# Performance work log

Measured on AMD Instinct MI355X. Metric: run time of the kernel, lower is better.

Reference implementation:

```python
import jax, jax.numpy as jnp
import numpy as np

N_NODES = 8192
N_GRAPHS = 16
KNN_K = 80
N_FEAT = 6
KNN_COLS = (0, 1, 2, 3)
HID = 128
HID6 = 6 * HID
N_LABELS = 3
BN_EPS = 1e-5


def knn_edges(pos, batch, k):
    # pos: [N, 4]; batch: [N] graph ids. Returns (src, tgt) with k neighbors per node,
    # restricted to same graph, excluding self (PyG knn_graph, flow source_to_target).
    n = pos.shape[0]
    sq = jnp.sum(pos * pos, axis=1)
    d2 = sq[:, None] + sq[None, :] - 2.0 * (pos @ pos.T)  # [N, N]
    valid = (batch[:, None] == batch[None, :]) & ~jnp.eye(n, dtype=bool)
    d2 = jnp.where(valid, d2, jnp.inf)
    _, idx = jax.lax.top_k(-d2, k)  # k smallest distances per row
    src = idx.reshape(-1)                      # neighbor j (message source)
    tgt = jnp.repeat(jnp.arange(n), k)         # center node i (message target)
    return src, tgt


def tag_conv(x, src, tgt, norm, W, b):
    # TAGConv K=2: out = sum_k (A_hat^k x) W_k + b, A_hat = D^-1/2 A D^-1/2
    n = x.shape[0]
    out = x @ W[0]
    h = x
    for k in range(1, W.shape[0]):
        h = jax.ops.segment_sum(norm[:, None] * h[src], tgt, num_segments=n)
        out = out + h @ W[k]
    return out + b


def pool_mean_max(x, batch, n_graphs):
    cnt = jax.ops.segment_sum(jnp.ones((x.shape[0],), x.dtype), batch, num_segments=n_graphs)
    mean = jax.ops.segment_sum(x, batch, num_segments=n_graphs) / cnt[:, None]
    mx = jax.ops.segment_max(x, batch, num_segments=n_graphs)
    return jnp.concatenate([mean, mx], axis=1)


def setup_inputs() -> dict:
    key = jax.random.key(0)
    ks = jax.random.split(key, 16)
    x = jax.random.normal(ks[0], (N_NODES, N_FEAT), dtype=jnp.float32)
    batch = jnp.repeat(jnp.arange(N_GRAPHS, dtype=jnp.int32), N_NODES // N_GRAPHS)
    s1 = 1.0 / np.sqrt(N_FEAT)
    s2 = 1.0 / np.sqrt(HID)
    s3 = 1.0 / np.sqrt(HID6)
    return {
        "x": x,
        "batch": batch,
        "conv1_w": jax.random.uniform(ks[1], (3, N_FEAT, HID), jnp.float32, -s1, s1),
        "conv1_b": jnp.zeros((HID,), jnp.float32),
        "conv2_w": jax.random.uniform(ks[2], (3, HID, HID), jnp.float32, -s2, s2),
        "conv2_b": jnp.zeros((HID,), jnp.float32),
        "conv3_w": jax.random.uniform(ks[3], (3, HID, HID), jnp.float32, -s2, s2),
        "conv3_b": jnp.zeros((HID,), jnp.float32),
        "bn_gamma": jnp.ones((HID6,), jnp.float32),
        "bn_beta": jnp.zeros((HID6,), jnp.float32),
        "bn_mean": 0.1 * jax.random.normal(ks[4], (HID6,), jnp.float32),
        "bn_var": jax.random.uniform(ks[5], (HID6,), jnp.float32, 0.5, 1.5),
        "lin_w": jax.random.uniform(ks[6], (5, HID6, HID6), jnp.float32, -s3, s3),
        "lin_b": jax.random.uniform(ks[7], (5, HID6), jnp.float32, -s3, s3),
        "out_w": jax.random.uniform(ks[8], (HID6, N_LABELS), jnp.float32, -s3, s3),
        "out_b": jax.random.uniform(ks[9], (N_LABELS,), jnp.float32, -s3, s3),
    }


def reference(x, batch, conv1_w, conv1_b, conv2_w, conv2_b, conv3_w, conv3_b,
              bn_gamma, bn_beta, bn_mean, bn_var, lin_w, lin_b, out_w, out_b):
    n = x.shape[0]
    pos = x[:, jnp.array(KNN_COLS)]
    src, tgt = knn_edges(pos, batch, KNN_K)
    # gcn_norm without self loops (edge dropout disabled: eval-mode determinism)
    deg = jax.ops.segment_sum(jnp.ones_like(src, dtype=x.dtype), tgt, num_segments=n)
    dinv = jnp.where(deg > 0, jax.lax.rsqrt(jnp.maximum(deg, 1.0)), 0.0)
    norm = dinv[src] * dinv[tgt]

    h = jax.nn.leaky_relu(tag_conv(x, src, tgt, norm, conv1_w, conv1_b))
    p1 = pool_mean_max(h, batch, N_GRAPHS)
    h = jax.nn.leaky_relu(tag_conv(h, src, tgt, norm, conv2_w, conv2_b))
    p2 = pool_mean_max(h, batch, N_GRAPHS)
    h = jax.nn.leaky_relu(tag_conv(h, src, tgt, norm, conv3_w, conv3_b))
    p3 = pool_mean_max(h, batch, N_GRAPHS)

    g = jnp.concatenate([p1, p2, p3], axis=1)  # [B, 768]
    g = (g - bn_mean) * jax.lax.rsqrt(bn_var + BN_EPS) * bn_gamma + bn_beta
    for i in range(lin_w.shape[0]):
        g = jax.nn.leaky_relu(g @ lin_w[i] + lin_b[i])
    out = g @ out_w + out_b
    return out.reshape(-1, N_LABELS)
```

## Files before the change

kernel.cpp:

```cpp
#include <hip/hip_runtime.h>

constexpr int N    = 8192;
constexpr int NPG  = 512;
constexpr int NG   = 16;
constexpr int KNN  = 80;
constexpr int F0   = 6;
constexpr int HID  = 128;
constexpr int H6   = 768;
constexpr int RPB  = 16;
constexpr int BPGR = NPG / RPB;


__device__ __forceinline__ float leaky(float v) { return v > 0.0f ? v : 0.01f * v; }

__device__ __forceinline__ int lanes_below(unsigned long long m) {
    return __builtin_amdgcn_mbcnt_hi((unsigned)(m >> 32),
           __builtin_amdgcn_mbcnt_lo((unsigned)m, 0));
}

__device__ __forceinline__ int wave_count_sum(int c) {
    int total = 0;
    #pragma unroll
    for (int b = 0; b < 4; b++)
        total += (int)__popcll(__ballot((c >> b) & 1)) << b;
    return total;
}

__global__ __launch_bounds__(256) void knn_kernel(const float* __restrict__ x,
                                                  int* __restrict__ nbr) {
    const int bid   = blockIdx.x;
    const int slot  = bid & 7;
    const int idx   = bid >> 3;
    const int g     = slot + 8 * (idx >> 7);
    const int chunk = idx & 127;
    const int tid  = threadIdx.x;
    const int lane = tid & 63;
    const int wv   = tid >> 6;
    const int base = g << 9;
    const int tl   = chunk * 4 + wv;
    const int t    = base + tl;

    __shared__ float px[512], py[512], pz[512], pw[512];
    __shared__ unsigned long long skey[4 * 128];

    for (int j = tid; j < 512; j += 256) {
        const float* row = x + (size_t)(base + j) * F0;
        const float2 ra = *(const float2*)(row);
        const float2 rb = *(const float2*)(row + 2);
        px[j] = ra.x; py[j] = ra.y; pz[j] = rb.x; pw[j] = rb.y;
    }
    __syncthreads();

    const float tx = px[tl], ty = py[tl], tz = pz[tl], tw = pw[tl];
    const float sqt = tx*tx + ty*ty + tz*tz + tw*tw;

    unsigned d2m[8];
    #pragma unroll
    for (int j = 0; j < 8; j++) {
        const int node = j * 64 + lane;
        const float jx = px[node], jy = py[node], jz = pz[node], jw = pw[node];
        const float sqj = jx*jx + jy*jy + jz*jz + jw*jw;
        const float dot = tx*jx + ty*jy + tz*jz + tw*jw;
        const float d2  = sqt + sqj - 2.0f * dot;
        unsigned u = __float_as_uint(d2);
        u = (u & 0x80000000u) ? ~u : (u | 0x80000000u);
        d2m[j] = (node == tl) ? 0xFFFFFFFFu : u;
    }

    unsigned V = 0;
    for (int b = 31; b >= 0; --b) {
        const unsigned test = V | (1u << b);
        int c = 0;
        #pragma unroll
        for (int j = 0; j < 8; j++) c += (d2m[j] < test) ? 1 : 0;
        if (wave_count_sum(c) < KNN) V = test;
    }

    int c = 0;
    #pragma unroll
    for (int j = 0; j < 8; j++) c += (d2m[j] < V) ? 1 : 0;
    const int n_lt = wave_count_sum(c);
    const int need = KNN - n_lt;

    const int woff = wv * 128;
    int cnt_total = 0, taken = 0;
    #pragma unroll
    for (int j = 0; j < 8; j++) {
        const bool lt = d2m[j] < V;
        const bool eq = d2m[j] == V;
        const unsigned long long meq = __ballot(eq);
        const bool sel = lt || (eq && (taken + lanes_below(meq)) < need);
        taken += (int)__popcll(meq);
        const unsigned long long msel = __ballot(sel);
        if (sel) {
            const int pos = cnt_total + lanes_below(msel);
            skey[woff + pos] = ((unsigned long long)d2m[j] << 32)
                             | (unsigned)(base + j * 64 + lane);
        }
        cnt_total += (int)__popcll(msel);
    }
    for (int i = KNN + lane; i < 128; i += 64) skey[woff + i] = ~0ULL;
    __syncthreads();

    for (int kk = 2; kk <= 128; kk <<= 1) {
        for (int jj = kk >> 1; jj >= 1; jj >>= 1) {
            const int i  = ((lane & ~(jj - 1)) << 1) | (lane & (jj - 1));
            const int ix = i | jj;
            const unsigned long long a = skey[woff + i];
            const unsigned long long b = skey[woff + ix];
            const bool up = ((i & kk) == 0);
            if ((a > b) == up) { skey[woff + i] = b; skey[woff + ix] = a; }
            __syncthreads();
        }
    }

    if (lane < KNN)      nbr[t * KNN + lane]      = (int)(unsigned)skey[woff + lane];
    if (lane + 64 < KNN) nbr[t * KNN + lane + 64] = (int)(unsigned)skey[woff + lane + 64];
}

__global__ __launch_bounds__(256) void prop6(const float* __restrict__ hin,
                                             const int* __restrict__ nbr,
                                             float* __restrict__ hout) {
    const int bid   = blockIdx.x;
    const int slot  = bid & 7;
    const int idx   = bid >> 3;
    const int g     = slot + 8 * (idx >> 4);
    const int chunk = idx & 15;
    const int t     = (g << 9) + chunk * 32 + (threadIdx.x >> 3);
    const int sl    = threadIdx.x & 7;
    const int* nb   = nbr + t * KNN + sl * 10;

    float a[F0] = {0.f, 0.f, 0.f, 0.f, 0.f, 0.f};
    #pragma unroll
    for (int j = 0; j < 10; j++) {
        const float* r = hin + (size_t)nb[j] * F0;
        #pragma unroll
        for (int f = 0; f < F0; f++) a[f] += r[f];
    }
    #pragma unroll
    for (int off = 1; off < 8; off <<= 1)
        #pragma unroll
        for (int f = 0; f < F0; f++) a[f] += __shfl_xor(a[f], off);

    if (sl == 0) {
        const float inv = 1.0f / 80.0f;
        float* o = hout + (size_t)t * F0;
        #pragma unroll
        for (int f = 0; f < F0; f++) o[f] = a[f] * inv;
    }
}

__global__ __launch_bounds__(256) void prop128(const float* __restrict__ hin,
                                               const int* __restrict__ nbr,
                                               float* __restrict__ hout) {
    const int bid   = blockIdx.x;
    const int slot  = bid & 7;
    const int g     = slot + (bid >> 9) * 8;
    const int chunk = (bid >> 3) & 63;
    const int lane  = threadIdx.x & 31;
    const int t     = (g << 9) + chunk * 8 + (threadIdx.x >> 5);
    const int* nb   = nbr + t * KNN;
    float a0=0.f,a1=0.f,a2=0.f,a3=0.f;
    for (int i = 0; i < KNN; i += 16) {
        const int4 sA = *(const int4*)(nb + i);
        const int4 sB = *(const int4*)(nb + i + 4);
        const int4 sC = *(const int4*)(nb + i + 8);
        const int4 sD = *(const int4*)(nb + i + 12);
        const int idx[16] = {sA.x,sA.y,sA.z,sA.w, sB.x,sB.y,sB.z,sB.w,
                             sC.x,sC.y,sC.z,sC.w, sD.x,sD.y,sD.z,sD.w};
        float4 v[16];
        #pragma unroll
        for (int q = 0; q < 16; q++)
            v[q] = *(const float4*)(hin + (size_t)idx[q] * HID + lane * 4);
        #pragma unroll
        for (int q = 0; q < 16; q += 4) {
            a0 += (v[q].x + v[q+1].x) + (v[q+2].x + v[q+3].x);
            a1 += (v[q].y + v[q+1].y) + (v[q+2].y + v[q+3].y);
            a2 += (v[q].z + v[q+1].z) + (v[q+2].z + v[q+3].z);
            a3 += (v[q].w + v[q+1].w) + (v[q+2].w + v[q+3].w);
        }
    }
    const float inv = 1.0f / 80.0f;
    float4 r; r.x=a0*inv; r.y=a1*inv; r.z=a2*inv; r.w=a3*inv;
    *(float4*)(hout + (size_t)t * HID + lane * 4) = r;
}

__global__ __launch_bounds__(256) void combine6(const float* __restrict__ X,
                                                const float* __restrict__ Y1,
                                                const float* __restrict__ Y2,
                                                const float* __restrict__ W,
                                                const float* __restrict__ bias,
                                                float* __restrict__ out,
                                                float* __restrict__ psum,
                                                float* __restrict__ pmax) {
    constexpr int K = F0;
    __shared__ float xs[3][RPB * K];
    const int bid   = blockIdx.x;
    const int slot  = bid & 7;
    const int idx   = bid >> 3;
    const int g     = slot + 8 * (idx >> 5);
    const int tile  = g * BPGR + (idx & 31);
    const int row0  = tile * RPB;
    const int tid   = threadIdx.x;

    for (int i = tid; i < RPB * K; i += 256) xs[0][i] = X [(size_t)row0 * K + i];
    for (int i = tid; i < RPB * K; i += 256) xs[1][i] = Y1[(size_t)row0 * K + i];
    for (int i = tid; i < RPB * K; i += 256) xs[2][i] = Y2[(size_t)row0 * K + i];
    __syncthreads();

    const int c  = tid & 127;
    const int r0 = (tid >> 7) * 8;

    float acc[8];
    #pragma unroll
    for (int r = 0; r < 8; r++) acc[r] = 0.0f;

    #pragma unroll
    for (int s = 0; s < 3; s++) {
        const float* __restrict__ Ws   = W + (size_t)s * K * HID;
        const float* __restrict__ xseg = xs[s] + r0 * K;
        #pragma unroll
        for (int k = 0; k < K; k++) {
            const float w0 = Ws[(size_t)k * HID + c];
            #pragma unroll
            for (int r = 0; r < 8; r++)
                acc[r] += xseg[r * K + k] * w0;
        }
    }

    const float bb = bias[c];
    float sum8 = 0.0f, mx8 = -3.402823e38f;
    #pragma unroll
    for (int r = 0; r < 8; r++) {
        const float v = leaky(acc[r] + bb);
        out[(size_t)(row0 + r0 + r) * HID + c] = v;
        sum8 += v;
        mx8 = fmaxf(mx8, v);
    }

    __shared__ float ssum[128], smx[128];
    if (r0) { ssum[c] = sum8; smx[c] = mx8; }
    __syncthreads();
    if (!r0) {
        psum[(size_t)tile * HID + c] = sum8 + ssum[c];
        pmax[(size_t)tile * HID + c] = fmaxf(mx8, smx[c]);
    }
}

__global__ __launch_bounds__(256) void combine128f(const float* __restrict__ X,
                                                   const float* __restrict__ Y1,
                                                   const int* __restrict__ nbr,
                                                   const float* __restrict__ W,
                                                   const float* __restrict__ bias,
                                                   float* __restrict__ out,
                                                   float* __restrict__ psum,
                                                   float* __restrict__ pmax) {
    constexpr int K = HID;
    __shared__ float xs[3][RPB * K];
    const int bid   = blockIdx.x;
    const int slot  = bid & 7;
    const int idx   = bid >> 3;
    const int g     = slot + (idx >> 5) * 8;
    const int chunk = idx & 31;
    const int tile  = g * BPGR + chunk;
    const int row0  = tile * RPB;
    const int tid   = threadIdx.x;

    {
        const float* s0 = X  + (size_t)row0 * K;
        const float* s1 = Y1 + (size_t)row0 * K;
        constexpr int NV = RPB * K / 4;
        for (int i = tid; i < NV; i += 256) ((float4*)xs[0])[i] = ((const float4*)s0)[i];
        for (int i = tid; i < NV; i += 256) ((float4*)xs[1])[i] = ((const float4*)s1)[i];
    }
    {
        const int lane = tid & 31;
        const int w8   = tid >> 5;
        const float inv = 1.0f / 80.0f;
        #pragma unroll
        for (int rr = 0; rr < 2; rr++) {
            const int r = w8 + rr * 8;
            const int* nb = nbr + (size_t)(row0 + r) * KNN;
            float a0=0.f,a1=0.f,a2=0.f,a3=0.f;
            for (int i = 0; i < KNN; i += 16) {
                const int4 sA = *(const int4*)(nb + i);
                const int4 sB = *(const int4*)(nb + i + 4);
                const int4 sC = *(const int4*)(nb + i + 8);
                const int4 sD = *(const int4*)(nb + i + 12);
                const int ix[16] = {sA.x,sA.y,sA.z,sA.w, sB.x,sB.y,sB.z,sB.w,
                                    sC.x,sC.y,sC.z,sC.w, sD.x,sD.y,sD.z,sD.w};
                float4 v[16];
                #pragma unroll
                for (int q = 0; q < 16; q++)
                    v[q] = *(const float4*)(Y1 + (size_t)ix[q] * HID + lane * 4);
                #pragma unroll
                for (int q = 0; q < 16; q += 4) {
                    a0 += (v[q].x + v[q+1].x) + (v[q+2].x + v[q+3].x);
                    a1 += (v[q].y + v[q+1].y) + (v[q+2].y + v[q+3].y);
                    a2 += (v[q].z + v[q+1].z) + (v[q+2].z + v[q+3].z);
                    a3 += (v[q].w + v[q+1].w) + (v[q+2].w + v[q+3].w);
                }
            }
            float4 o; o.x=a0*inv; o.y=a1*inv; o.z=a2*inv; o.w=a3*inv;
            *(float4*)&xs[2][r * K + lane * 4] = o;
        }
    }
    __syncthreads();

    const int c  = tid & 127;
    const int r0 = (tid >> 7) * 8;

    float acc[8];
    #pragma unroll
    for (int r = 0; r < 8; r++) acc[r] = 0.0f;

    #pragma unroll
    for (int s = 0; s < 3; s++) {
        const float* __restrict__ Ws   = W + (size_t)s * K * HID;
        const float* __restrict__ xseg = xs[s] + r0 * K;
        for (int k = 0; k < K; k += 2) {
            const float w0 = Ws[(size_t)k * HID + c];
            const float w1 = Ws[(size_t)(k + 1) * HID + c];
            #pragma unroll
            for (int r = 0; r < 8; r++)
                acc[r] += xseg[r * K + k] * w0 + xseg[r * K + k + 1] * w1;
        }
    }

    const float bb = bias[c];
    float sum8 = 0.0f, mx8 = -3.402823e38f;
    #pragma unroll
    for (int r = 0; r < 8; r++) {
        const float v = leaky(acc[r] + bb);
        out[(size_t)(row0 + r0 + r) * HID + c] = v;
        sum8 += v;
        mx8 = fmaxf(mx8, v);
    }

    __shared__ float ssum[128], smx[128];
    if (r0) { ssum[c] = sum8; smx[c] = mx8; }
    __syncthreads();
    if (!r0) {
        psum[(size_t)tile * HID + c] = sum8 + ssum[c];
        pmax[(size_t)tile * HID + c] = fmaxf(mx8, smx[c]);
    }
}

__global__ __launch_bounds__(256) void lin0_kernel(const float* __restrict__ psum1,
                                                   const float* __restrict__ pmax1,
                                                   const float* __restrict__ psum2,
                                                   const float* __restrict__ pmax2,
                                                   const float* __restrict__ psum3,
                                                   const float* __restrict__ pmax3,
                                                   const float* __restrict__ gamma,
                                                   const float* __restrict__ beta,
                                                   const float* __restrict__ mean,
                                                   const float* __restrict__ var,
                                                   const float* __restrict__ W,
                                                   const float* __restrict__ bias,
                                                   float* __restrict__ gout) {
    const int r   = blockIdx.x / 6;
    const int cc  = blockIdx.x % 6;
    const int tid = threadIdx.x;

    __shared__ float gs[H6];
    {
        const int cv = tid >> 7;
        const int c  = tid & 127;
        const float* ps = (cv ? psum2 : psum1) + (size_t)r * BPGR * HID + c;
        const float* pm = (cv ? pmax2 : pmax1) + (size_t)r * BPGR * HID + c;
        float s = 0.0f, m = -3.402823e38f;
        #pragma unroll 8
        for (int b = 0; b < BPGR; b++) { s += ps[b * HID]; m = fmaxf(m, pm[b * HID]); }
        gs[cv * 256 + c]       = s * (1.0f / 512.0f);
        gs[cv * 256 + 128 + c] = m;
    }
    if (tid < 128) {
        const float* ps = psum3 + (size_t)r * BPGR * HID + tid;
        const float* pm = pmax3 + (size_t)r * BPGR * HID + tid;
        float s = 0.0f, m = -3.402823e38f;
        #pragma unroll 8
        for (int b = 0; b < BPGR; b++) { s += ps[b * HID]; m = fmaxf(m, pm[b * HID]); }
        gs[512 + tid]       = s * (1.0f / 512.0f);
        gs[512 + 128 + tid] = m;
    }
    __syncthreads();
    for (int k = tid; k < H6; k += 256)
        gs[k] = (gs[k] - mean[k]) * (1.0f / sqrtf(var[k] + 1e-5f)) * gamma[k] + beta[k];
    __syncthreads();

    const int c  = cc * 128 + (tid & 127);
    const int kh = tid >> 7;
    const int kb = kh * 384;
    float a0=0.f,a1=0.f,a2=0.f,a3=0.f;
    for (int k = kb; k < kb + 384; k += 4) {
        a0 += gs[k]     * W[(size_t)(k)     * H6 + c];
        a1 += gs[k + 1] * W[(size_t)(k + 1) * H6 + c];
        a2 += gs[k + 2] * W[(size_t)(k + 2) * H6 + c];
        a3 += gs[k + 3] * W[(size_t)(k + 3) * H6 + c];
    }
    __shared__ float part[256];
    part[tid] = (a0 + a1) + (a2 + a3);
    __syncthreads();
    if (kh == 0) {
        const float v = part[tid] + part[tid + 128] + bias[c];
        gout[(size_t)r * H6 + c] = leaky(v);
    }
}

__global__ __launch_bounds__(256) void lin_kernel(const float* __restrict__ gin,
                                                  const float* __restrict__ W,
                                                  const float* __restrict__ bias,
                                                  float* __restrict__ gout) {
    const int r   = blockIdx.x / 6;
    const int cc  = blockIdx.x % 6;
    const int tid = threadIdx.x;

    __shared__ float gs[H6];
    for (int k = tid; k < H6; k += 256) gs[k] = gin[(size_t)r * H6 + k];
    __syncthreads();

    const int c  = cc * 128 + (tid & 127);
    const int kh = tid >> 7;
    const int kb = kh * 384;
    float a0=0.f,a1=0.f,a2=0.f,a3=0.f;
    for (int k = kb; k < kb + 384; k += 4) {
        a0 += gs[k]     * W[(size_t)(k)     * H6 + c];
        a1 += gs[k + 1] * W[(size_t)(k + 1) * H6 + c];
        a2 += gs[k + 2] * W[(size_t)(k + 2) * H6 + c];
        a3 += gs[k + 3] * W[(size_t)(k + 3) * H6 + c];
    }
    __shared__ float part[256];
    part[tid] = (a0 + a1) + (a2 + a3);
    __syncthreads();
    if (kh == 0) {
        const float v = part[tid] + part[tid + 128] + bias[c];
        gout[(size_t)r * H6 + c] = leaky(v);
    }
}

__global__ void out_kernel(const float* __restrict__ gin,
                           const float* __restrict__ W,
                           const float* __restrict__ bias,
                           float* __restrict__ out) {
    const int tid = threadIdx.x;
    __shared__ float part[192];
    if (tid < 192) {
        const int q  = tid >> 2;
        const int r  = q / 3, c = q % 3;
        const int kq = tid & 3;
        float acc = 0.0f;
        for (int k = kq * 192; k < kq * 192 + 192; k++)
            acc += gin[(size_t)r * H6 + k] * W[(size_t)k * 3 + c];
        part[tid] = acc;
    }
    __syncthreads();
    if (tid < 48) {
        const int r = tid / 3, c = tid % 3;
        out[r * 3 + c] = part[tid*4] + part[tid*4+1] + part[tid*4+2] + part[tid*4+3] + bias[c];
    }
}

extern "C" void kernel_launch(void* const* d_in, const int* in_sizes, int n_in,
                              void* d_out, int out_size, void* d_ws, size_t ws_size,
                              hipStream_t stream) {
    const float* x        = (const float*)d_in[0];
    const float* conv1_w  = (const float*)d_in[2];
    const float* conv1_b  = (const float*)d_in[3];
    const float* conv2_w  = (const float*)d_in[4];
    const float* conv2_b  = (const float*)d_in[5];
    const float* conv3_w  = (const float*)d_in[6];
    const float* conv3_b  = (const float*)d_in[7];
    const float* bn_gamma = (const float*)d_in[8];
    const float* bn_beta  = (const float*)d_in[9];
    const float* bn_mean  = (const float*)d_in[10];
    const float* bn_var   = (const float*)d_in[11];
    const float* lin_w    = (const float*)d_in[12];
    const float* lin_b    = (const float*)d_in[13];
    const float* out_w    = (const float*)d_in[14];
    const float* out_b    = (const float*)d_in[15];

    char* ws = (char*)d_ws;
    size_t off = 0;
    auto alloc = [&](size_t bytes) {
        void* p = ws + off;
        off += (bytes + 255) & ~(size_t)255;
        return p;
    };
    int*   nbr   = (int*)  alloc((size_t)N * KNN * 4);
    float* y6a   = (float*)alloc((size_t)N * F0 * 4);
    float* y6b   = (float*)alloc((size_t)N * F0 * 4);
    float* hA    = (float*)alloc((size_t)N * HID * 4);
    float* hB    = (float*)alloc((size_t)N * HID * 4);
    float* y1    = (float*)alloc((size_t)N * HID * 4);
    float* ga    = (float*)alloc((size_t)NG * H6 * 4);
    float* gb    = (float*)alloc((size_t)NG * H6 * 4);
    float* psum1 = (float*)alloc((size_t)(N / RPB) * HID * 4);
    float* pmax1 = (float*)alloc((size_t)(N / RPB) * HID * 4);
    float* psum2 = (float*)alloc((size_t)(N / RPB) * HID * 4);
    float* pmax2 = (float*)alloc((size_t)(N / RPB) * HID * 4);
    float* psum3 = (float*)alloc((size_t)(N / RPB) * HID * 4);
    float* pmax3 = (float*)alloc((size_t)(N / RPB) * HID * 4);

    knn_kernel<<<N / 4, 256, 0, stream>>>(x, nbr);

    prop6<<<N * 8 / 256, 256, 0, stream>>>(x, nbr, y6a);
    prop6<<<N * 8 / 256, 256, 0, stream>>>(y6a, nbr, y6b);
    combine6<<<N / RPB, 256, 0, stream>>>(x, y6a, y6b, conv1_w, conv1_b, hA, psum1, pmax1);

    prop128<<<N / 8, 256, 0, stream>>>(hA, nbr, y1);
    combine128f<<<N / RPB, 256, 0, stream>>>(hA, y1, nbr, conv2_w, conv2_b, hB, psum2, pmax2);

    prop128<<<N / 8, 256, 0, stream>>>(hB, nbr, y1);
    combine128f<<<N / RPB, 256, 0, stream>>>(hB, y1, nbr, conv3_w, conv3_b, hA, psum3, pmax3);

    lin0_kernel<<<96, 256, 0, stream>>>(psum1, pmax1, psum2, pmax2, psum3, pmax3,
                                        bn_gamma, bn_beta, bn_mean, bn_var,
                                        lin_w + 0 * H6 * H6, lin_b + 0 * H6, gb);
    lin_kernel<<<96, 256, 0, stream>>>(gb, lin_w + 1 * H6 * H6, lin_b + 1 * H6, ga);
    lin_kernel<<<96, 256, 0, stream>>>(ga, lin_w + 2 * H6 * H6, lin_b + 2 * H6, gb);
    lin_kernel<<<96, 256, 0, stream>>>(gb, lin_w + 3 * H6 * H6, lin_b + 3 * H6, ga);
    lin_kernel<<<96, 256, 0, stream>>>(ga, lin_w + 4 * H6 * H6, lin_b + 4 * H6, gb);
    out_kernel<<<1, 256, 0, stream>>>(gb, out_w, out_b, (float*)d_out);
}
```

Before: 248.2 us.

## Replace neighbor gathers with dense per-graph bitmask propagation

New measurement: 431.1 us. 1.74x slower.

```diff
diff --git a/kernel.cpp b/kernel.cpp
--- a/kernel.cpp
+++ b/kernel.cpp
@@ -10,7 +10,6 @@
 constexpr int RPB  = 16;
 constexpr int BPGR = NPG / RPB;
 
-
 __device__ __forceinline__ float leaky(float v) { return v > 0.0f ? v : 0.01f * v; }
 
 __device__ __forceinline__ int lanes_below(unsigned long long m) {
@@ -27,7 +26,8 @@
 }
 
 __global__ __launch_bounds__(256) void knn_kernel(const float* __restrict__ x,
-                                                  int* __restrict__ nbr) {
+                                                  int* __restrict__ nbr,
+                                                  unsigned* __restrict__ mask) {
     const int bid   = blockIdx.x;
     const int slot  = bid & 7;
     const int idx   = bid >> 3;
@@ -42,6 +42,7 @@
 
     __shared__ float px[512], py[512], pz[512], pw[512];
     __shared__ unsigned long long skey[4 * 128];
+    __shared__ unsigned msk[4][16];
 
     for (int j = tid; j < 512; j += 256) {
         const float* row = x + (size_t)(base + j) * F0;
@@ -114,8 +115,20 @@
         }
     }
 
-    if (lane < KNN)      nbr[t * KNN + lane]      = (int)(unsigned)skey[woff + lane];
-    if (lane + 64 < KNN) nbr[t * KNN + lane + 64] = (int)(unsigned)skey[woff + lane + 64];
+    if (lane < 16) msk[wv][lane] = 0u;
+    __syncthreads();
+    if (lane < KNN) {
+        const int idxn = (int)(unsigned)skey[woff + lane];
+        nbr[t * KNN + lane] = idxn;
+        atomicOr(&msk[wv][(idxn & 511) >> 5], 1u << (idxn & 31));
+    }
+    if (lane + 64 < KNN) {
+        const int idxn = (int)(unsigned)skey[woff + lane + 64];
+        nbr[t * KNN + lane + 64] = idxn;
+        atomicOr(&msk[wv][(idxn & 511) >> 5], 1u << (idxn & 31));
+    }
+    __syncthreads();
+    if (lane < 16) mask[(size_t)t * 16 + lane] = msk[wv][lane];
 }
 
 __global__ __launch_bounds__(256) void prop6(const float* __restrict__ hin,
@@ -150,39 +163,43 @@
     }
 }
 
-__global__ __launch_bounds__(256) void prop128(const float* __restrict__ hin,
-                                               const int* __restrict__ nbr,
-                                               float* __restrict__ hout) {
+__global__ __launch_bounds__(256) void prop_dense(const float* __restrict__ H,
+                                                  const unsigned* __restrict__ mask,
+                                                  float* __restrict__ Y) {
     const int bid   = blockIdx.x;
     const int slot  = bid & 7;
-    const int g     = slot + (bid >> 9) * 8;
-    const int chunk = (bid >> 3) & 63;
-    const int lane  = threadIdx.x & 31;
-    const int t     = (g << 9) + chunk * 8 + (threadIdx.x >> 5);
-    const int* nb   = nbr + t * KNN;
-    float a0=0.f,a1=0.f,a2=0.f,a3=0.f;
-    for (int i = 0; i < KNN; i += 16) {
-        const int4 sA = *(const int4*)(nb + i);
-        const int4 sB = *(const int4*)(nb + i + 4);
-        const int4 sC = *(const int4*)(nb + i + 8);
-        const int4 sD = *(const int4*)(nb + i + 12);
-        const int idx[16] = {sA.x,sA.y,sA.z,sA.w, sB.x,sB.y,sB.z,sB.w,
-                             sC.x,sC.y,sC.z,sC.w, sD.x,sD.y,sD.z,sD.w};
-        float4 v[16];
-        #pragma unroll
-        for (int q = 0; q < 16; q++)
-            v[q] = *(const float4*)(hin + (size_t)idx[q] * HID + lane * 4);
-        #pragma unroll
-        for (int q = 0; q < 16; q += 4) {
-            a0 += (v[q].x + v[q+1].x) + (v[q+2].x + v[q+3].x);
-            a1 += (v[q].y + v[q+1].y) + (v[q+2].y + v[q+3].y);
-            a2 += (v[q].z + v[q+1].z) + (v[q+2].z + v[q+3].z);
-            a3 += (v[q].w + v[q+1].w) + (v[q+2].w + v[q+3].w);
+    const int idx   = bid >> 3;
+    const int g     = slot + 8 * (idx >> 5);
+    const int chunk = idx & 31;
+    const int tid   = threadIdx.x;
+    const int tsub  = tid >> 4;
+    const int c0    = (tid & 15) * 8;
+    const int t     = (g << 9) + chunk * 16 + tsub;
+    const unsigned* __restrict__ mrow = mask + (size_t)t * 16;
+    const float* __restrict__ hbase = H + ((size_t)(g << 9)) * HID + c0;
+
+    float acc[8] = {0.f,0.f,0.f,0.f,0.f,0.f,0.f,0.f};
+    for (int w = 0; w < 16; ++w) {
+        const unsigned word = mrow[w];
+        const float* hp = hbase + (size_t)(w * 32) * HID;
+        #pragma unroll 4
+        for (int b = 0; b < 32; ++b) {
+            const float bit = (float)((word >> b) & 1u);
+            const float4 v0 = *(const float4*)(hp);
+            const float4 v1 = *(const float4*)(hp + 4);
+            acc[0] += bit * v0.x; acc[1] += bit * v0.y;
+            acc[2] += bit * v0.z; acc[3] += bit * v0.w;
+            acc[4] += bit * v1.x; acc[5] += bit * v1.y;
+            acc[6] += bit * v1.z; acc[7] += bit * v1.w;
+            hp += HID;
         }
     }
     const float inv = 1.0f / 80.0f;
-    float4 r; r.x=a0*inv; r.y=a1*inv; r.z=a2*inv; r.w=a3*inv;
-    *(float4*)(hout + (size_t)t * HID + lane * 4) = r;
+    float* yp = Y + (size_t)t * HID + c0;
+    float4 o0 = { acc[0]*inv, acc[1]*inv, acc[2]*inv, acc[3]*inv };
+    float4 o1 = { acc[4]*inv, acc[5]*inv, acc[6]*inv, acc[7]*inv };
+    *(float4*)(yp)     = o0;
+    *(float4*)(yp + 4) = o1;
 }
 
 __global__ __launch_bounds__(256) void combine6(const float* __restrict__ X,
@@ -247,63 +264,32 @@
     }
 }
 
-__global__ __launch_bounds__(256) void combine128f(const float* __restrict__ X,
-                                                   const float* __restrict__ Y1,
-                                                   const int* __restrict__ nbr,
-                                                   const float* __restrict__ W,
-                                                   const float* __restrict__ bias,
-                                                   float* __restrict__ out,
-                                                   float* __restrict__ psum,
-                                                   float* __restrict__ pmax) {
+__global__ __launch_bounds__(256) void combine128(const float* __restrict__ X,
+                                                  const float* __restrict__ Y1,
+                                                  const float* __restrict__ Y2,
+                                                  const float* __restrict__ W,
+                                                  const float* __restrict__ bias,
+                                                  float* __restrict__ out,
+                                                  float* __restrict__ psum,
+                                                  float* __restrict__ pmax) {
     constexpr int K = HID;
     __shared__ float xs[3][RPB * K];
     const int bid   = blockIdx.x;
     const int slot  = bid & 7;
     const int idx   = bid >> 3;
     const int g     = slot + (idx >> 5) * 8;
-    const int chunk = idx & 31;
-    const int tile  = g * BPGR + chunk;
+    const int tile  = g * BPGR + (idx & 31);
     const int row0  = tile * RPB;
     const int tid   = threadIdx.x;
 
     {
         const float* s0 = X  + (size_t)row0 * K;
         const float* s1 = Y1 + (size_t)row0 * K;
+        const float* s2 = Y2 + (size_t)row0 * K;
         constexpr int NV = RPB * K / 4;
         for (int i = tid; i < NV; i += 256) ((float4*)xs[0])[i] = ((const float4*)s0)[i];
         for (int i = tid; i < NV; i += 256) ((float4*)xs[1])[i] = ((const float4*)s1)[i];
-    }
-    {
-        const int lane = tid & 31;
-        const int w8   = tid >> 5;
-        const float inv = 1.0f / 80.0f;
-        #pragma unroll
-        for (int rr = 0; rr < 2; rr++) {
-            const int r = w8 + rr * 8;
-            const int* nb = nbr + (size_t)(row0 + r) * KNN;
-            float a0=0.f,a1=0.f,a2=0.f,a3=0.f;
-            for (int i = 0; i < KNN; i += 16) {
-                const int4 sA = *(const int4*)(nb + i);
-                const int4 sB = *(const int4*)(nb + i + 4);
-                const int4 sC = *(const int4*)(nb + i + 8);
-                const int4 sD = *(const int4*)(nb + i + 12);
-                const int ix[16] = {sA.x,sA.y,sA.z,sA.w, sB.x,sB.y,sB.z,sB.w,
-                                    sC.x,sC.y,sC.z,sC.w, sD.x,sD.y,sD.z,sD.w};
-                float4 v[16];
-                #pragma unroll
-                for (int q = 0; q < 16; q++)
-                    v[q] = *(const float4*)(Y1 + (size_t)ix[q] * HID + lane * 4);
-                #pragma unroll
-                for (int q = 0; q < 16; q += 4) {
-                    a0 += (v[q].x + v[q+1].x) + (v[q+2].x + v[q+3].x);
-                    a1 += (v[q].y + v[q+1].y) + (v[q+2].y + v[q+3].y);
-                    a2 += (v[q].z + v[q+1].z) + (v[q+2].z + v[q+3].z);
-                    a3 += (v[q].w + v[q+1].w) + (v[q+2].w + v[q+3].w);
-                }
-            }
-            float4 o; o.x=a0*inv; o.y=a1*inv; o.z=a2*inv; o.w=a3*inv;
-            *(float4*)&xs[2][r * K + lane * 4] = o;
-        }
+        for (int i = tid; i < NV; i += 256) ((float4*)xs[2])[i] = ((const float4*)s2)[i];
     }
     __syncthreads();
 
@@ -487,32 +473,36 @@
         off += (bytes + 255) & ~(size_t)255;
         return p;
     };
-    int*   nbr   = (int*)  alloc((size_t)N * KNN * 4);
-    float* y6a   = (float*)alloc((size_t)N * F0 * 4);
-    float* y6b   = (float*)alloc((size_t)N * F0 * 4);
-    float* hA    = (float*)alloc((size_t)N * HID * 4);
-    float* hB    = (float*)alloc((size_t)N * HID * 4);
-    float* y1    = (float*)alloc((size_t)N * HID * 4);
-    float* ga    = (float*)alloc((size_t)NG * H6 * 4);
-    float* gb    = (float*)alloc((size_t)NG * H6 * 4);
-    float* psum1 = (float*)alloc((size_t)(N / RPB) * HID * 4);
-    float* pmax1 = (float*)alloc((size_t)(N / RPB) * HID * 4);
-    float* psum2 = (float*)alloc((size_t)(N / RPB) * HID * 4);
-    float* pmax2 = (float*)alloc((size_t)(N / RPB) * HID * 4);
-    float* psum3 = (float*)alloc((size_t)(N / RPB) * HID * 4);
-    float* pmax3 = (float*)alloc((size_t)(N / RPB) * HID * 4);
-
-    knn_kernel<<<N / 4, 256, 0, stream>>>(x, nbr);
+    int*      nbr   = (int*)     alloc((size_t)N * KNN * 4);
+    unsigned* mask  = (unsigned*)alloc((size_t)N * 16 * 4);
+    float*    y6a   = (float*)   alloc((size_t)N * F0 * 4);
+    float*    y6b   = (float*)   alloc((size_t)N * F0 * 4);
+    float*    hA    = (float*)   alloc((size_t)N * HID * 4);
+    float*    hB    = (float*)   alloc((size_t)N * HID * 4);
+    float*    y1    = (float*)   alloc((size_t)N * HID * 4);
+    float*    y2    = (float*)   alloc((size_t)N * HID * 4);
+    float*    ga    = (float*)   alloc((size_t)NG * H6 * 4);
+    float*    gb    = (float*)   alloc((size_t)NG * H6 * 4);
+    float*    psum1 = (float*)   alloc((size_t)(N / RPB) * HID * 4);
+    float*    pmax1 = (float*)   alloc((size_t)(N / RPB) * HID * 4);
+    float*    psum2 = (float*)   alloc((size_t)(N / RPB) * HID * 4);
+    float*    pmax2 = (float*)   alloc((size_t)(N / RPB) * HID * 4);
+    float*    psum3 = (float*)   alloc((size_t)(N / RPB) * HID * 4);
+    float*    pmax3 = (float*)   alloc((size_t)(N / RPB) * HID * 4);
+
+    knn_kernel<<<N / 4, 256, 0, stream>>>(x, nbr, mask);
 
     prop6<<<N * 8 / 256, 256, 0, stream>>>(x, nbr, y6a);
     prop6<<<N * 8 / 256, 256, 0, stream>>>(y6a, nbr, y6b);
     combine6<<<N / RPB, 256, 0, stream>>>(x, y6a, y6b, conv1_w, conv1_b, hA, psum1, pmax1);
 
-    prop128<<<N / 8, 256, 0, stream>>>(hA, nbr, y1);
-    combine128f<<<N / RPB, 256, 0, stream>>>(hA, y1, nbr, conv2_w, conv2_b, hB, psum2, pmax2);
-
-    prop128<<<N / 8, 256, 0, stream>>>(hB, nbr, y1);
-    combine128f<<<N / RPB, 256, 0, stream>>>(hB, y1, nbr, conv3_w, conv3_b, hA, psum3, pmax3);
+    prop_dense<<<512, 256, 0, stream>>>(hA, mask, y1);
+    prop_dense<<<512, 256, 0, stream>>>(y1, mask, y2);
+    combine128<<<N / RPB, 256, 0, stream>>>(hA, y1, y2, conv2_w, conv2_b, hB, psum2, pmax2);
+
+    prop_dense<<<512, 256, 0, stream>>>(hB, mask, y1);
+    prop_dense<<<512, 256, 0, stream>>>(y1, mask, y2);
+    combine128<<<N / RPB, 256, 0, stream>>>(hB, y1, y2, conv3_w, conv3_b, hA, psum3, pmax3);
 
     lin0_kernel<<<96, 256, 0, stream>>>(psum1, pmax1, psum2, pmax2, psum3, pmax3,
                                         bn_gamma, bn_beta, bn_mean, bn_var,
```

## Reorder prop128 target nodes by first coordinate for gather locality

Applied to the files above, without the earlier changes.

Result: slower. 259.2 us (+4.4%).

```diff
diff --git a/kernel.cpp b/kernel.cpp
--- a/kernel.cpp
+++ b/kernel.cpp
@@ -9,7 +9,6 @@
 constexpr int H6   = 768;
 constexpr int RPB  = 16;
 constexpr int BPGR = NPG / RPB;
-
 
 __device__ __forceinline__ float leaky(float v) { return v > 0.0f ? v : 0.01f * v; }
 
@@ -118,6 +117,77 @@
     if (lane + 64 < KNN) nbr[t * KNN + lane + 64] = (int)(unsigned)skey[woff + lane + 64];
 }
 
+__global__ __launch_bounds__(256) void sortperm_kernel(const float* __restrict__ x,
+                                                       int* __restrict__ perm) {
+    __shared__ unsigned long long key[512];
+    const int g    = blockIdx.x;
+    const int base = g << 9;
+    const int tid  = threadIdx.x;
+
+    for (int j = tid; j < 512; j += 256) {
+        unsigned u = __float_as_uint(x[(size_t)(base + j) * F0]);
+        u = (u & 0x80000000u) ? ~u : (u | 0x80000000u);
+        key[j] = ((unsigned long long)u << 32) | (unsigned)j;
+    }
+    __syncthreads();
+
+    for (int kk = 2; kk <= 512; kk <<= 1) {
+        for (int jj = kk >> 1; jj > 0; jj >>= 1) {
+            #pragma unroll
+            for (int rep = 0; rep < 2; rep++) {
+                const int i  = tid + rep * 256;
+                const int ix = i ^ jj;
+                if (ix > i) {
+                    const unsigned long long a = key[i], b = key[ix];
+                    const bool up = ((i & kk) == 0);
+                    if ((a > b) == up) { key[i] = b; key[ix] = a; }
+                }
+            }
+            __syncthreads();
+        }
+    }
+
+    for (int j = tid; j < 512; j += 256)
+        perm[base + j] = (int)(key[j] & 511u);
+}
+
+__global__ __launch_bounds__(256) void prop128(const float* __restrict__ hin,
+                                               const int* __restrict__ nbr,
+                                               const int* __restrict__ perm,
+                                               float* __restrict__ hout) {
+    const int bid   = blockIdx.x;
+    const int slot  = bid & 7;
+    const int g     = slot + (bid >> 9) * 8;
+    const int chunk = (bid >> 3) & 63;
+    const int lane  = threadIdx.x & 31;
+    const int base  = g << 9;
+    const int t     = base + perm[base + chunk * 8 + (threadIdx.x >> 5)];
+    const int* nb   = nbr + t * KNN;
+    float a0=0.f,a1=0.f,a2=0.f,a3=0.f;
+    for (int i = 0; i < KNN; i += 16) {
+        const int4 sA = *(const int4*)(nb + i);
+        const int4 sB = *(const int4*)(nb + i + 4);
+        const int4 sC = *(const int4*)(nb + i + 8);
+        const int4 sD = *(const int4*)(nb + i + 12);
+        const int idx[16] = {sA.x,sA.y,sA.z,sA.w, sB.x,sB.y,sB.z,sB.w,
+                             sC.x,sC.y,sC.z,sC.w, sD.x,sD.y,sD.z,sD.w};
+        float4 v[16];
+        #pragma unroll
+        for (int q = 0; q < 16; q++)
+            v[q] = *(const float4*)(hin + (size_t)idx[q] * HID + lane * 4);
+        #pragma unroll
+        for (int q = 0; q < 16; q += 4) {
+            a0 += (v[q].x + v[q+1].x) + (v[q+2].x + v[q+3].x);
+            a1 += (v[q].y + v[q+1].y) + (v[q+2].y + v[q+3].y);
+            a2 += (v[q].z + v[q+1].z) + (v[q+2].z + v[q+3].z);
+            a3 += (v[q].w + v[q+1].w) + (v[q+2].w + v[q+3].w);
+        }
+    }
+    const float inv = 1.0f / 80.0f;
+    float4 r; r.x=a0*inv; r.y=a1*inv; r.z=a2*inv; r.w=a3*inv;
+    *(float4*)(hout + (size_t)t * HID + lane * 4) = r;
+}
+
 __global__ __launch_bounds__(256) void prop6(const float* __restrict__ hin,
                                              const int* __restrict__ nbr,
                                              float* __restrict__ hout) {
@@ -148,41 +218,6 @@
         #pragma unroll
         for (int f = 0; f < F0; f++) o[f] = a[f] * inv;
     }
-}
-
-__global__ __launch_bounds__(256) void prop128(const float* __restrict__ hin,
-                                               const int* __restrict__ nbr,
-                                               float* __restrict__ hout) {
-    const int bid   = blockIdx.x;
-    const int slot  = bid & 7;
-    const int g     = slot + (bid >> 9) * 8;
-    const int chunk = (bid >> 3) & 63;
-    const int lane  = threadIdx.x & 31;
-    const int t     = (g << 9) + chunk * 8 + (threadIdx.x >> 5);
-    const int* nb   = nbr + t * KNN;
-    float a0=0.f,a1=0.f,a2=0.f,a3=0.f;
-    for (int i = 0; i < KNN; i += 16) {
-        const int4 sA = *(const int4*)(nb + i);
-        const int4 sB = *(const int4*)(nb + i + 4);
-        const int4 sC = *(const int4*)(nb + i + 8);
-        const int4 sD = *(const int4*)(nb + i + 12);
-        const int idx[16] = {sA.x,sA.y,sA.z,sA.w, sB.x,sB.y,sB.z,sB.w,
-                             sC.x,sC.y,sC.z,sC.w, sD.x,sD.y,sD.z,sD.w};
-        float4 v[16];
-        #pragma unroll
-        for (int q = 0; q < 16; q++)
-            v[q] = *(const float4*)(hin + (size_t)idx[q] * HID + lane * 4);
-        #pragma unroll
-        for (int q = 0; q < 16; q += 4) {
-            a0 += (v[q].x + v[q+1].x) + (v[q+2].x + v[q+3].x);
-            a1 += (v[q].y + v[q+1].y) + (v[q+2].y + v[q+3].y);
-            a2 += (v[q].z + v[q+1].z) + (v[q+2].z + v[q+3].z);
-            a3 += (v[q].w + v[q+1].w) + (v[q+2].w + v[q+3].w);
-        }
-    }
-    const float inv = 1.0f / 80.0f;
-    float4 r; r.x=a0*inv; r.y=a1*inv; r.z=a2*inv; r.w=a3*inv;
-    *(float4*)(hout + (size_t)t * HID + lane * 4) = r;
 }
 
 __global__ __launch_bounds__(256) void combine6(const float* __restrict__ X,
@@ -488,6 +523,7 @@
         return p;
     };
     int*   nbr   = (int*)  alloc((size_t)N * KNN * 4);
+    int*   perm  = (int*)  alloc((size_t)N * 4);
     float* y6a   = (float*)alloc((size_t)N * F0 * 4);
     float* y6b   = (float*)alloc((size_t)N * F0 * 4);
     float* hA    = (float*)alloc((size_t)N * HID * 4);
@@ -503,15 +539,16 @@
     float* pmax3 = (float*)alloc((size_t)(N / RPB) * HID * 4);
 
     knn_kernel<<<N / 4, 256, 0, stream>>>(x, nbr);
+    sortperm_kernel<<<NG, 256, 0, stream>>>(x, perm);
 
     prop6<<<N * 8 / 256, 256, 0, stream>>>(x, nbr, y6a);
     prop6<<<N * 8 / 256, 256, 0, stream>>>(y6a, nbr, y6b);
     combine6<<<N / RPB, 256, 0, stream>>>(x, y6a, y6b, conv1_w, conv1_b, hA, psum1, pmax1);
 
-    prop128<<<N / 8, 256, 0, stream>>>(hA, nbr, y1);
+    prop128<<<N / 8, 256, 0, stream>>>(hA, nbr, perm, y1);
     combine128f<<<N / RPB, 256, 0, stream>>>(hA, y1, nbr, conv2_w, conv2_b, hB, psum2, pmax2);
 
-    prop128<<<N / 8, 256, 0, stream>>>(hB, nbr, y1);
+    prop128<<<N / 8, 256, 0, stream>>>(hB, nbr, perm, y1);
     combine128f<<<N / RPB, 256, 0, stream>>>(hB, y1, nbr, conv3_w, conv3_b, hA, psum3, pmax3);
 
     lin0_kernel<<<96, 256, 0, stream>>>(psum1, pmax1, psum2, pmax2, psum3, pmax3,
```
